# Kernel optimization log

Hardware: AMD Instinct MI355X
Metric: run time of the kernel (lower is better)

The kernel has to match this reference:

```python
import jax, jax.numpy as jnp
import numpy as np

K = 5          # number of neighbors (self excluded)
EPS = 1e-7     # distance epsilon
Q = 0.98       # quantile for radius normalization


def _cdist(A):
    # Euclidean pairwise distances [N, N] via the matmul expansion.
    sq = jnp.sum(A * A, axis=-1)
    d2 = sq[:, None] + sq[None, :] - 2.0 * (A @ A.T)
    return jnp.sqrt(jnp.maximum(d2, 0.0))


def _lid(values):
    # values: [N, K] ascending neighbor distances; LID via log-distance ratios.
    norm = values[:, -1:]
    return -jnp.sum(jnp.log10(values) - jnp.log10(norm), axis=1)


def setup_inputs() -> dict:
    key = jax.random.key(0)
    k1, k2 = jax.random.split(key)
    X = jax.random.normal(k1, (8192, 256), dtype=jnp.float32)
    Z = jax.random.normal(k2, (8192, 64), dtype=jnp.float32)
    return {"X": X, "Z": Z}


def reference(X, Z):
    n = X.shape[0]
    normA1 = jnp.quantile(jnp.linalg.norm(X - jnp.mean(X, axis=0), axis=1), Q)
    normA2 = jnp.quantile(jnp.linalg.norm(Z - jnp.mean(Z, axis=0), axis=1), Q)

    # k-NN in X space (drop self at column 0)
    x_dist = (_cdist(X) + EPS) / normA1
    neg_vals, idx = jax.lax.top_k(-x_dist, K + 1)   # smallest K+1, ascending
    values = (-neg_vals)[:, 1:]
    nn_mask = idx[:, 1:]
    lid_X = _lid(values)

    # gather the SAME neighbor indices in Z space
    z_dist = (_cdist(Z) + EPS) / normA2
    extracted = jnp.take_along_axis(z_dist, nn_mask, axis=1)
    lid_Z = _lid(extracted)

    return jnp.sum(jnp.square(lid_X - lid_Z)) / (n * K * 10)
```

## Files before the change

### kernel.cpp

```cpp
#include <hip/hip_runtime.h>
#include <math.h>
#include <stdint.h>

#define EPS     1e-7f
#define NR      8192
#define DX      256
#define DZ      64
#define KNN     5
#define KEEP    6
#define NSPLIT  8
#define NPOOL   (NSPLIT * KEEP)
#define NCAND   16
#define JS      (NR / NSPLIT)
#define JT      64
#define NCHUNK  (JS / JT)
#define RBLK    64
#define SC1     0x7F7F7F7F
#define BIASF   256.0f

typedef float f32x4 __attribute__((ext_vector_type(4)));
typedef int   i32x8 __attribute__((ext_vector_type(8)));

__device__ __forceinline__ uint32_t umin_(uint32_t a, uint32_t b) {
    return __builtin_elementwise_min(a, b);
}
__device__ __forceinline__ uint32_t umax_(uint32_t a, uint32_t b) {
    return __builtin_elementwise_max(a, b);
}

__device__ __forceinline__ uint32_t to_e4m3(float f) {
    const uint32_t u = __float_as_uint(f);
    const uint32_t s = (u >> 24) & 0x80u;
    const int e = (int)((u >> 23) & 0xFFu) - 127;
    if (e < -10) return s;
    if (e > 8)   return s | 0x7Eu;
    const uint32_t mant = (u & 0x7FFFFFu) | 0x800000u;
    const int shift = (e < -6) ? (14 - e) : 20;
    uint32_t q = (mant + (1u << (shift - 1))) >> shift;
    int E = (e < -6) ? 0 : (e + 7);
    if (q >= 16) { q >>= 1; E += 1; }
    if (E == 0) return s | q;
    return s | ((uint32_t)E << 3) | (q & 7u);
}

__global__ __launch_bounds__(256) void split_k(const float* __restrict__ X,
                                               uint8_t* __restrict__ Xq,
                                               float* __restrict__ sqX,
                                               float* __restrict__ out) {
    if (blockIdx.x == 0 && threadIdx.x == 0) out[0] = 0.0f;
    const int row  = blockIdx.x * 4 + (threadIdx.x >> 6);
    const int lane = threadIdx.x & 63;
    const float4 v = *(const float4*)&X[(size_t)row * DX + lane * 4];
    float s = v.x * v.x + v.y * v.y + v.z * v.z + v.w * v.w;
    const uint32_t b = to_e4m3(v.x) | (to_e4m3(v.y) << 8) |
                       (to_e4m3(v.z) << 16) | (to_e4m3(v.w) << 24);
    ((uint32_t*)Xq)[(size_t)row * (DX / 4) + lane] = b;
    #pragma unroll
    for (int o = 32; o > 0; o >>= 1) s += __shfl_down(s, o);
    if (lane == 0) sqX[row] = s;
}

#define FOLD_BODY(KILL)                                                                   \
    _Pragma("unroll")                                                                     \
    for (int g = 0; g < 2; ++g) {                                                         \
        _Pragma("unroll")                                                                 \
        for (int r = 0; r < 4; ++r) {                                                     \
            const int q = g * 4 + r;                                                      \
            uint32_t c0 = (__float_as_uint(acc[0][g][r]) & 0xFFFFE000u) | (uint32_t)j0;   \
            uint32_t c1 = (__float_as_uint(acc[1][g][r]) & 0xFFFFE000u) | (uint32_t)j1;   \
            if (KILL) {                                                                   \
                const int irow = rowbase + g * 16 + quad * 4 + r;                         \
                c0 = (j0 == irow) ? 0xFFFFFFFFu : c0;                                     \
                c1 = (j1 == irow) ? 0xFFFFFFFFu : c1;                                     \
            }                                                                             \
            const uint32_t lo = umin_(c0, c1);                                            \
            const uint32_t hi = umax_(c0, c1);                                            \
            const uint32_t b0 = best[q][0], b1 = best[q][1], b2 = best[q][2],             \
                           b3 = best[q][3];                                               \
            best[q][0] = umin_(b0, lo);                                                   \
            best[q][1] = umin_(umin_(b1, hi), umax_(b0, lo));                             \
            best[q][2] = umin_(umin_(b2, umax_(b1, lo)), umax_(b0, hi));                  \
            best[q][3] = umin_(umin_(b3, umax_(b2, lo)), umax_(b1, hi));                  \
        }                                                                                 \
    }

#define STAGE(t) do {                                                                     \
    uint8_t* const _base = &smem[(t) & 1][0];                                             \
    _Pragma("unroll")                                                                     \
    for (int u = 0; u < 4; ++u) {                                                         \
        __builtin_amdgcn_global_load_lds(                                                 \
            (const __attribute__((address_space(1))) uint32_t*)srcp[u],                   \
            (__attribute__((address_space(3))) uint32_t*)(_base + dstoff[u]),             \
            16, 0, 0);                                                                    \
        srcp[u] += JT * DX;                                                               \
    }                                                                                     \
} while (0)

__global__ __launch_bounds__(256, 2) void mfma_topk_k(const uint8_t* __restrict__ Xq,
                                                      const float* __restrict__ sqX,
                                                      uint32_t* __restrict__ partials) {
    __shared__ __align__(16) uint8_t smem[2][16384];
    __shared__ uint32_t mb2[RBLK][2][KNN];
    __shared__ __align__(16) float sq_s[JS];

    const int tid  = threadIdx.x;
    const int w    = tid >> 6;
    const int lane = tid & 63;
    const int n    = lane & 15;
    const int quad = lane >> 4;
    const int x7   = n & 7;
    const int h    = w >> 1;
    const int sp   = w & 1;
    const int s    = blockIdx.x & 7;
    const int ib   = (blockIdx.x >> 3) * RBLK;
    const int jb0  = s * JS;
    const int rowbase = ib + h * 32;

    ((f32x4*)sq_s)[tid] = ((const f32x4*)(sqX + jb0))[tid];

    const int rel   = rowbase - jb0;
    const int cdiag = __builtin_amdgcn_readfirstlane((rel >= 0 && rel < JS) ? (rel >> 6) : -1);

    i32x8 Aq[2][2];
    #pragma unroll
    for (int g = 0; g < 2; ++g)
        #pragma unroll
        for (int kf = 0; kf < 2; ++kf)
            Aq[g][kf] = *(const i32x8*)(Xq + (size_t)(rowbase + g * 16 + n) * DX
                                        + kf * 128 + quad * 32);

    uint32_t best[8][4];
    #pragma unroll
    for (int q = 0; q < 8; ++q)
        #pragma unroll
        for (int k = 0; k < 4; ++k) best[q][k] = 0xFFFFFFFFu;

    const uint8_t* srcp[4];
    int            dstoff[4];
    #pragma unroll
    for (int u = 0; u < 4; ++u) {
        const int q  = w * 256 + u * 64 + lane;
        const int sj = q >> 4;
        const int c  = (q & 15) ^ (sj & 7);
        srcp[u]   = Xq + (size_t)jb0 * DX + sj * DX + c * 16;
        dstoff[u] = (w * 256 + u * 64) * 16;
    }
    int bidx[2][2][2];
    #pragma unroll
    for (int kf = 0; kf < 2; ++kf)
        #pragma unroll
        for (int si = 0; si < 2; ++si) {
            const int sj = (sp * 2 + si) * 16 + n;
            const int cb = kf * 8 + quad * 2;
            bidx[kf][si][0] = sj * 16 + (cb ^ x7);
            bidx[kf][si][1] = sj * 16 + ((cb + 1) ^ x7);
        }
    const float* sqp = sq_s + sp * 32 + n;
    int j0 = jb0 + sp * 32 + n;

    STAGE(0);

    for (int jc = 0; jc < NCHUNK; ++jc) {
        __syncthreads();
        if (jc + 1 < NCHUNK) STAGE(jc + 1);
        const uint4* Bv = (const uint4*)&smem[jc & 1][0];

        const float ini0 = fmaf(-0.5f, sqp[jc * JT],      -BIASF);
        const float ini1 = fmaf(-0.5f, sqp[jc * JT + 16], -BIASF);

        f32x4 acc[2][2];
        #pragma unroll
        for (int g = 0; g < 2; ++g)
            #pragma unroll
            for (int r = 0; r < 4; ++r) { acc[0][g][r] = ini0; acc[1][g][r] = ini1; }

        #pragma unroll
        for (int kf = 0; kf < 2; ++kf) {
            #pragma unroll
            for (int si = 0; si < 2; ++si) {
                union { uint4 p[2]; i32x8 v; } bb;
                bb.p[0] = Bv[bidx[kf][si][0]];
                bb.p[1] = Bv[bidx[kf][si][1]];
                acc[si][0] = __builtin_amdgcn_mfma_scale_f32_16x16x128_f8f6f4(
                                 Aq[0][kf], bb.v, acc[si][0], 0, 0, 0, SC1, 0, SC1);
                acc[si][1] = __builtin_amdgcn_mfma_scale_f32_16x16x128_f8f6f4(
                                 Aq[1][kf], bb.v, acc[si][1], 0, 0, 0, SC1, 0, SC1);
            }
        }

        const int j1 = j0 + 16;
        if (jc != cdiag) {
            FOLD_BODY(0)
        } else {
            FOLD_BODY(1)
        }
        j0 += JT;
    }

    #pragma unroll
    for (int q = 0; q < 8; ++q) {
        const uint32_t s0 = best[q][0], s1 = best[q][1], s2 = best[q][2], s3 = best[q][3];
        const uint32_t t0 = __shfl_xor(s0, 1);
        const uint32_t t1 = __shfl_xor(s1, 1);
        const uint32_t t2 = __shfl_xor(s2, 1);
        const uint32_t t3 = __shfl_xor(s3, 1);
        uint32_t a0 = umin_(s0, t0);
        uint32_t a1 = umin_(umin_(s1, t1), umax_(s0, t0));
        uint32_t a2 = umin_(umin_(s2, t2), umin_(umax_(s1, t0), umax_(s0, t1)));
        uint32_t a3 = umin_(umin_(s3, t3),
                            umin_(umax_(s2, t0), umin_(umax_(s1, t1), umax_(s0, t2))));
        uint32_t a4 = umin_(umin_(umax_(s3, t0), umax_(s2, t1)),
                            umin_(umax_(s1, t2), umax_(s0, t3)));
        #pragma unroll
        for (int mask = 2; mask <= 8; mask <<= 1) {
            const uint32_t b0 = __shfl_xor(a0, mask);
            const uint32_t b1 = __shfl_xor(a1, mask);
            const uint32_t b2 = __shfl_xor(a2, mask);
            const uint32_t b3 = __shfl_xor(a3, mask);
            const uint32_t b4 = __shfl_xor(a4, mask);
            const uint32_t c0 = umin_(a0, b0);
            const uint32_t c1 = umin_(umin_(a1, b1), umax_(a0, b0));
            const uint32_t c2 = umin_(umin_(a2, b2), umin_(umax_(a0, b1), umax_(a1, b0)));
            const uint32_t c3 = umin_(umin_(a3, b3),
                                      umin_(umax_(a1, b1), umin_(umax_(a0, b2), umax_(a2, b0))));
            const uint32_t c4 = umin_(umin_(a4, b4),
                                      umin_(umin_(umax_(a0, b3), umax_(a1, b2)),
                                            umin_(umax_(a2, b1), umax_(a3, b0))));
            a0 = c0; a1 = c1; a2 = c2; a3 = c3; a4 = c4;
        }
        const int rloc = h * 32 + (q >> 2) * 16 + quad * 4 + (q & 3);
        uint32_t v = a0;
        v = (n == 1) ? a1 : v;
        v = (n == 2) ? a2 : v;
        v = (n == 3) ? a3 : v;
        v = (n == 4) ? a4 : v;
        if (n < KNN) mb2[rloc][sp][n] = v;
    }
    __syncthreads();

    if (tid < RBLK) {
        const uint32_t a0 = mb2[tid][0][0], a1 = mb2[tid][0][1], a2 = mb2[tid][0][2],
                       a3 = mb2[tid][0][3], a4 = mb2[tid][0][4];
        const uint32_t b0 = mb2[tid][1][0], b1 = mb2[tid][1][1], b2 = mb2[tid][1][2],
                       b3 = mb2[tid][1][3], b4 = mb2[tid][1][4];
        uint32_t o[KEEP];
        o[0] = umin_(a0, b0);
        o[1] = umin_(umin_(a1, b1), umax_(a0, b0));
        o[2] = umin_(umin_(a2, b2), umin_(umax_(a0, b1), umax_(a1, b0)));
        o[3] = umin_(umin_(a3, b3), umin_(umax_(a1, b1), umin_(umax_(a0, b2), umax_(a2, b0))));
        o[4] = umin_(umin_(a4, b4), umin_(umin_(umax_(a0, b3), umax_(a1, b2)),
                                          umin_(umax_(a2, b1), umax_(a3, b0))));
        o[5] = umin_(umin_(umax_(a0, b4), umax_(a4, b0)),
                     umin_(umax_(a1, b3), umin_(umax_(a2, b2), umax_(a3, b1))));
        #pragma unroll
        for (int k = 0; k < KEEP; ++k)
            partials[(size_t)(ib + tid) * NPOOL + s * KEEP + k] = o[k];
    }
}

__global__ __launch_bounds__(256) void finalize_k(const uint32_t* __restrict__ parts,
                                                  const float* __restrict__ X,
                                                  const float* __restrict__ Z,
                                                  const float* __restrict__ sqX,
                                                  float* __restrict__ out) {
    __shared__ float wsum[4];
    const int wv   = threadIdx.x >> 6;
    const int lane = threadIdx.x & 63;
    const int i    = blockIdx.x * 4 + wv;

    uint32_t v = (lane < NPOOL) ? parts[(size_t)i * NPOOL + lane] : 0xFFFFFFFFu;
    #pragma unroll
    for (int kk = 2; kk <= 64; kk <<= 1) {
        #pragma unroll
        for (int jj = kk >> 1; jj > 0; jj >>= 1) {
            const uint32_t o = __shfl_xor(v, jj);
            const bool keepmin = ((lane & kk) == 0) == ((lane & jj) == 0);
            v = keepmin ? umin_(v, o) : umax_(v, o);
        }
    }

    const float4 xi = *(const float4*)(X + (size_t)i * DX + lane * 4);

    float p[16];
    #pragma unroll
    for (int c = 0; c < NCAND; ++c) {
        const int jc = (int)(__shfl(v, c) & 0x1FFFu);
        const float4 xj = *(const float4*)(X + (size_t)jc * DX + lane * 4);
        p[c] = fmaf(xi.x, xj.x, fmaf(xi.y, xj.y, fmaf(xi.z, xj.z, xi.w * xj.w)));
    }
    #pragma unroll
    for (int c = 0; c < NCAND; ++c) {
        p[c] += __shfl_xor(p[c], 1);
        p[c] += __shfl_xor(p[c], 2);
        p[c] += __shfl_xor(p[c], 4);
        p[c] += __shfl_xor(p[c], 8);
    }
    const int cs = lane & 15;
    float dotv = p[0];
    dotv = (cs == 1)  ? p[1]  : dotv;
    dotv = (cs == 2)  ? p[2]  : dotv;
    dotv = (cs == 3)  ? p[3]  : dotv;
    dotv = (cs == 4)  ? p[4]  : dotv;
    dotv = (cs == 5)  ? p[5]  : dotv;
    dotv = (cs == 6)  ? p[6]  : dotv;
    dotv = (cs == 7)  ? p[7]  : dotv;
    dotv = (cs == 8)  ? p[8]  : dotv;
    dotv = (cs == 9)  ? p[9]  : dotv;
    dotv = (cs == 10) ? p[10] : dotv;
    dotv = (cs == 11) ? p[11] : dotv;
    dotv = (cs == 12) ? p[12] : dotv;
    dotv = (cs == 13) ? p[13] : dotv;
    dotv = (cs == 14) ? p[14] : dotv;
    dotv = (cs == 15) ? p[15] : dotv;
    dotv += __shfl_xor(dotv, 16);
    dotv += __shfl_xor(dotv, 32);

    unsigned long long k16 = 0xFFFFFFFFFFFFFFFFull;
    const int jl = (int)(v & 0x1FFFu);
    if (lane < NCAND) {
        const float d2x = (sqX[i] + sqX[jl]) - 2.0f * dotv;
        k16 = ((unsigned long long)__float_as_uint(d2x) << 32) | (unsigned)jl;
    }
    #pragma unroll
    for (int kk = 2; kk <= 16; kk <<= 1) {
        #pragma unroll
        for (int jj = kk >> 1; jj > 0; jj >>= 1) {
            const unsigned long long o = __shfl_xor(k16, jj);
            const bool keepmin = ((lane & kk) == 0) == ((lane & jj) == 0);
            k16 = keepmin ? (k16 < o ? k16 : o) : (k16 < o ? o : k16);
        }
    }

    const float d2k = __uint_as_float((uint32_t)(k16 >> 32));
    const int   jk  = (int)(k16 & 0x1FFFull);
    float lkx = 0.0f;
    if (lane < KNN) lkx = log10f(sqrtf(fmaxf(d2k, 0.0f)) + EPS);
    const float l4x = __shfl(lkx, KNN - 1);
    float sx = lkx;
    sx += __shfl_xor(sx, 1);
    sx += __shfl_xor(sx, 2);
    sx += __shfl_xor(sx, 4);

    const float zi = Z[(size_t)i * DZ + lane];
    float zsum = 0.0f, l4z = 0.0f;
    #pragma unroll
    for (int k = 0; k < KNN; ++k) {
        const int jz = __shfl(jk, k);
        const float zj = Z[(size_t)jz * DZ + lane];
        const float d = zi - zj;
        float s = d * d;
        s += __shfl_xor(s, 1);
        s += __shfl_xor(s, 2);
        s += __shfl_xor(s, 4);
        s += __shfl_xor(s, 8);
        s += __shfl_xor(s, 16);
        s += __shfl_xor(s, 32);
        const float lk = log10f(sqrtf(fmaxf(s, 0.0f)) + EPS);
        zsum += lk;
        if (k == KNN - 1) l4z = lk;
    }

    if (lane == 0) {
        const float lx = -(__shfl(sx, 0) - (float)KNN * l4x);
        const float lz = -(zsum - (float)KNN * l4z);
        const float diff = lx - lz;
        wsum[wv] = diff * diff * (1.0f / ((float)NR * KNN * 10.0f));
    }
    __syncthreads();
    if (threadIdx.x == 0)
        atomicAdd(out, wsum[0] + wsum[1] + wsum[2] + wsum[3]);
}

extern "C" void kernel_launch(void* const* d_in, const int* in_sizes, int n_in,
                              void* d_out, int out_size, void* d_ws, size_t ws_size,
                              hipStream_t stream) {
    const float* X = (const float*)d_in[0];
    const float* Z = (const float*)d_in[1];
    float* out = (float*)d_out;

    char* ws = (char*)d_ws;
    float*     sqX      = (float*)ws;
    uint32_t*  partials = (uint32_t*)(ws + 32768);
    uint8_t*   Xq       = (uint8_t*)(ws + 32768 + 2097152);

    split_k<<<NR / 4, 256, 0, stream>>>(X, Xq, sqX, out);
    mfma_topk_k<<<(NR / RBLK) * NSPLIT, 256, 0, stream>>>(Xq, sqX, partials);
    finalize_k<<<NR / 4, 256, 0, stream>>>(partials, X, Z, sqX, out);
}
```

Measured before the change: 136.5 us.

## Split row tile across 8 waves with 512-thread blocks in top-k kernel

The MFMA top-k kernel goes from 4 to 8 waves per block. Each wave now handles 16 rows instead of 32, so it issues one MFMA per B fragment instead of two and keeps half as many running top-k lists. The LDS staging work is spread across twice as many threads. This aims to add latency hiding through more waves per CU and to lower register pressure, at the cost of each B fragment loaded from LDS being reused by only one A tile per wave, which doubles LDS read traffic per MFMA.

```diff
diff --git a/kernel.cpp b/kernel.cpp
--- a/kernel.cpp
+++ b/kernel.cpp
@@ -18,8 +18,8 @@
 #define SC1     0x7F7F7F7F
 #define BIASF   256.0f
 
-typedef float f32x4 __attribute__((ext_vector_type(4)));
-typedef int   i32x8 __attribute__((ext_vector_type(8)));
+typedef float  f32x4 __attribute__((ext_vector_type(4)));
+typedef int    i32x8 __attribute__((ext_vector_type(8)));
 
 __device__ __forceinline__ uint32_t umin_(uint32_t a, uint32_t b) {
     return __builtin_elementwise_min(a, b);
@@ -62,32 +62,28 @@
 
 #define FOLD_BODY(KILL)                                                                   \
     _Pragma("unroll")                                                                     \
-    for (int g = 0; g < 2; ++g) {                                                         \
-        _Pragma("unroll")                                                                 \
-        for (int r = 0; r < 4; ++r) {                                                     \
-            const int q = g * 4 + r;                                                      \
-            uint32_t c0 = (__float_as_uint(acc[0][g][r]) & 0xFFFFE000u) | (uint32_t)j0;   \
-            uint32_t c1 = (__float_as_uint(acc[1][g][r]) & 0xFFFFE000u) | (uint32_t)j1;   \
-            if (KILL) {                                                                   \
-                const int irow = rowbase + g * 16 + quad * 4 + r;                         \
-                c0 = (j0 == irow) ? 0xFFFFFFFFu : c0;                                     \
-                c1 = (j1 == irow) ? 0xFFFFFFFFu : c1;                                     \
-            }                                                                             \
-            const uint32_t lo = umin_(c0, c1);                                            \
-            const uint32_t hi = umax_(c0, c1);                                            \
-            const uint32_t b0 = best[q][0], b1 = best[q][1], b2 = best[q][2],             \
-                           b3 = best[q][3];                                               \
-            best[q][0] = umin_(b0, lo);                                                   \
-            best[q][1] = umin_(umin_(b1, hi), umax_(b0, lo));                             \
-            best[q][2] = umin_(umin_(b2, umax_(b1, lo)), umax_(b0, hi));                  \
-            best[q][3] = umin_(umin_(b3, umax_(b2, lo)), umax_(b1, hi));                  \
+    for (int r = 0; r < 4; ++r) {                                                         \
+        uint32_t c0 = (__float_as_uint(acc[0][r]) & 0xFFFFE000u) | (uint32_t)j0;          \
+        uint32_t c1 = (__float_as_uint(acc[1][r]) & 0xFFFFE000u) | (uint32_t)j1;          \
+        if (KILL) {                                                                       \
+            const int irow = rowbase + quad * 4 + r;                                      \
+            c0 = (j0 == irow) ? 0xFFFFFFFFu : c0;                                         \
+            c1 = (j1 == irow) ? 0xFFFFFFFFu : c1;                                         \
         }                                                                                 \
+        const uint32_t lo = umin_(c0, c1);                                                \
+        const uint32_t hi = umax_(c0, c1);                                                \
+        const uint32_t b0 = best[r][0], b1 = best[r][1], b2 = best[r][2],                 \
+                       b3 = best[r][3];                                                   \
+        best[r][0] = umin_(b0, lo);                                                       \
+        best[r][1] = umin_(umin_(b1, hi), umax_(b0, lo));                                 \
+        best[r][2] = umin_(umin_(b2, umax_(b1, lo)), umax_(b0, hi));                      \
+        best[r][3] = umin_(umin_(b3, umax_(b2, lo)), umax_(b1, hi));                      \
     }
 
 #define STAGE(t) do {                                                                     \
     uint8_t* const _base = &smem[(t) & 1][0];                                             \
     _Pragma("unroll")                                                                     \
-    for (int u = 0; u < 4; ++u) {                                                         \
+    for (int u = 0; u < 2; ++u) {                                                         \
         __builtin_amdgcn_global_load_lds(                                                 \
             (const __attribute__((address_space(1))) uint32_t*)srcp[u],                   \
             (__attribute__((address_space(3))) uint32_t*)(_base + dstoff[u]),             \
@@ -96,7 +92,7 @@
     }                                                                                     \
 } while (0)
 
-__global__ __launch_bounds__(256, 2) void mfma_topk_k(const uint8_t* __restrict__ Xq,
+__global__ __launch_bounds__(512, 2) void mfma_topk_k(const uint8_t* __restrict__ Xq,
                                                       const float* __restrict__ sqX,
                                                       uint32_t* __restrict__ partials) {
     __shared__ __align__(16) uint8_t smem[2][16384];
@@ -114,36 +110,33 @@
     const int s    = blockIdx.x & 7;
     const int ib   = (blockIdx.x >> 3) * RBLK;
     const int jb0  = s * JS;
-    const int rowbase = ib + h * 32;
-
-    ((f32x4*)sq_s)[tid] = ((const f32x4*)(sqX + jb0))[tid];
+    const int rowbase = ib + h * 16;
+
+    ((float2*)sq_s)[tid] = ((const float2*)(sqX + jb0))[tid];
 
     const int rel   = rowbase - jb0;
     const int cdiag = __builtin_amdgcn_readfirstlane((rel >= 0 && rel < JS) ? (rel >> 6) : -1);
 
-    i32x8 Aq[2][2];
-    #pragma unroll
-    for (int g = 0; g < 2; ++g)
-        #pragma unroll
-        for (int kf = 0; kf < 2; ++kf)
-            Aq[g][kf] = *(const i32x8*)(Xq + (size_t)(rowbase + g * 16 + n) * DX
-                                        + kf * 128 + quad * 32);
-
-    uint32_t best[8][4];
-    #pragma unroll
-    for (int q = 0; q < 8; ++q)
-        #pragma unroll
-        for (int k = 0; k < 4; ++k) best[q][k] = 0xFFFFFFFFu;
-
-    const uint8_t* srcp[4];
-    int            dstoff[4];
-    #pragma unroll
-    for (int u = 0; u < 4; ++u) {
-        const int q  = w * 256 + u * 64 + lane;
+    i32x8 Aq[2];
+    #pragma unroll
+    for (int kf = 0; kf < 2; ++kf)
+        Aq[kf] = *(const i32x8*)(Xq + (size_t)(rowbase + n) * DX + kf * 128 + quad * 32);
+
+    uint32_t best[4][4];
+    #pragma unroll
+    for (int r = 0; r < 4; ++r)
+        #pragma unroll
+        for (int k = 0; k < 4; ++k) best[r][k] = 0xFFFFFFFFu;
+
+    const uint8_t* srcp[2];
+    int            dstoff[2];
+    #pragma unroll
+    for (int u = 0; u < 2; ++u) {
+        const int q  = w * 128 + u * 64 + lane;
         const int sj = q >> 4;
         const int c  = (q & 15) ^ (sj & 7);
         srcp[u]   = Xq + (size_t)jb0 * DX + sj * DX + c * 16;
-        dstoff[u] = (w * 256 + u * 64) * 16;
+        dstoff[u] = (w * 128 + u * 64) * 16;
     }
     int bidx[2][2][2];
     #pragma unroll
@@ -168,11 +161,9 @@
         const float ini0 = fmaf(-0.5f, sqp[jc * JT],      -BIASF);
         const float ini1 = fmaf(-0.5f, sqp[jc * JT + 16], -BIASF);
 
-        f32x4 acc[2][2];
-        #pragma unroll
-        for (int g = 0; g < 2; ++g)
-            #pragma unroll
-            for (int r = 0; r < 4; ++r) { acc[0][g][r] = ini0; acc[1][g][r] = ini1; }
+        f32x4 acc[2];
+        #pragma unroll
+        for (int r = 0; r < 4; ++r) { acc[0][r] = ini0; acc[1][r] = ini1; }
 
         #pragma unroll
         for (int kf = 0; kf < 2; ++kf) {
@@ -181,10 +172,8 @@
                 union { uint4 p[2]; i32x8 v; } bb;
                 bb.p[0] = Bv[bidx[kf][si][0]];
                 bb.p[1] = Bv[bidx[kf][si][1]];
-                acc[si][0] = __builtin_amdgcn_mfma_scale_f32_16x16x128_f8f6f4(
-                                 Aq[0][kf], bb.v, acc[si][0], 0, 0, 0, SC1, 0, SC1);
-                acc[si][1] = __builtin_amdgcn_mfma_scale_f32_16x16x128_f8f6f4(
-                                 Aq[1][kf], bb.v, acc[si][1], 0, 0, 0, SC1, 0, SC1);
+                acc[si] = __builtin_amdgcn_mfma_scale_f32_16x16x128_f8f6f4(
+                              Aq[kf], bb.v, acc[si], 0, 0, 0, SC1, 0, SC1);
             }
         }
 
@@ -198,7 +187,7 @@
     }
 
     #pragma unroll
-    for (int q = 0; q < 8; ++q) {
+    for (int q = 0; q < 4; ++q) {
         const uint32_t s0 = best[q][0], s1 = best[q][1], s2 = best[q][2], s3 = best[q][3];
         const uint32_t t0 = __shfl_xor(s0, 1);
         const uint32_t t1 = __shfl_xor(s1, 1);
@@ -228,7 +217,7 @@
                                             umin_(umax_(a2, b1), umax_(a3, b0))));
             a0 = c0; a1 = c1; a2 = c2; a3 = c3; a4 = c4;
         }
-        const int rloc = h * 32 + (q >> 2) * 16 + quad * 4 + (q & 3);
+        const int rloc = h * 16 + quad * 4 + q;
         uint32_t v = a0;
         v = (n == 1) ? a1 : v;
         v = (n == 2) ? a2 : v;
@@ -384,6 +373,6 @@
     uint8_t*   Xq       = (uint8_t*)(ws + 32768 + 2097152);
 
     split_k<<<NR / 4, 256, 0, stream>>>(X, Xq, sqX, out);
-    mfma_topk_k<<<(NR / RBLK) * NSPLIT, 256, 0, stream>>>(Xq, sqX, partials);
+    mfma_topk_k<<<(NR / RBLK) * NSPLIT, 512, 0, stream>>>(Xq, sqX, partials);
     finalize_k<<<NR / 4, 256, 0, stream>>>(partials, X, Z, sqX, out);
 }
```

After: 137.8 us. About the same (+0.9%).
